# Kernel tuning notes

Measured on AMD Instinct MI355X. Metric: run time of the kernel, lower is better.

## Reference

```python
import jax, jax.numpy as jnp
import numpy as np

COMMIT_WEIGHT = 0.25  # cfg.commit_weight


def setup_inputs() -> dict:
    key = jax.random.key(0)
    k1, k2 = jax.random.split(key)
    z = jax.random.normal(k1, (262144, 64), dtype=jnp.float32)
    codebook = jax.random.normal(k2, (512, 64), dtype=jnp.float32) * 0.02
    return {"z": z, "codebook": codebook}


def reference(z, codebook):
    # projector = Identity (apply_sim_vq=False)
    # squared euclidean distances [N, K]; argmin matches cdist(p=2) argmin
    d2 = (
        jnp.sum(z * z, axis=-1, keepdims=True)
        - 2.0 * (z @ codebook.T)
        + jnp.sum(codebook * codebook, axis=-1)
    )
    ids = jnp.argmin(d2, axis=-1)          # [N] int
    q = codebook[ids]                       # [N, D] gather
    loss = (
        jnp.mean((jax.lax.stop_gradient(z) - q) ** 2)
        + COMMIT_WEIGHT * jnp.mean((jax.lax.stop_gradient(q) - z) ** 2)
    )
    # straight-through estimator (training path)
    q_ste = z + jax.lax.stop_gradient(q - z)
    return q_ste, loss, ids
```

## Files before the change

kernel.cpp:

```cpp
#include <hip/hip_runtime.h>
#include <math.h>


constexpr int D     = 64;
constexpr int D4    = 16;
constexpr int K     = 512;
constexpr float STH = 2e-4f;

typedef __attribute__((ext_vector_type(8)))  short s16x8;
typedef __attribute__((ext_vector_type(16))) float f32x16;

#define FMA4(acc, zz, cc) do { \
  acc = fmaf((zz).x, (cc).x, acc); \
  acc = fmaf((zz).y, (cc).y, acc); \
  acc = fmaf((zz).z, (cc).z, acc); \
  acc = fmaf((zz).w, (cc).w, acc); } while (0)

#define MFMA_B(A, B, C) __builtin_amdgcn_mfma_f32_32x32x16_bf16(A, B, C, 0, 0, 0)

__device__ __forceinline__ unsigned short f2bf(float f) {
  unsigned u = __float_as_uint(f);
  return (unsigned short)((u + 0x7FFFu + ((u >> 16) & 1u)) >> 16);
}


#define LDS_FRAGS(CH, CL, T) do { \
  const int fb_ = (T) * 4096 + h * 512 + col * 16; \
  CH[0] = *(const s16x8*)(smem + fb_); \
  CH[1] = *(const s16x8*)(smem + fb_ + 1024); \
  CH[2] = *(const s16x8*)(smem + fb_ + 2048); \
  CH[3] = *(const s16x8*)(smem + fb_ + 3072); \
  CL[0] = *(const s16x8*)(smem + 65536 + fb_); \
  CL[1] = *(const s16x8*)(smem + 65536 + fb_ + 1024); \
  CL[2] = *(const s16x8*)(smem + 65536 + fb_ + 2048); \
  CL[3] = *(const s16x8*)(smem + 65536 + fb_ + 3072); \
} while (0)

#define LDS_GG(G, T) do { \
  const int gb_ = 131072 + (((T) * 32 + h * 16) << 2); \
  G[0] = *(const float4*)(smem + gb_); \
  G[1] = *(const float4*)(smem + gb_ + 16); \
  G[2] = *(const float4*)(smem + gb_ + 32); \
  G[3] = *(const float4*)(smem + gb_ + 48); \
} while (0)

#define TILE_BODY(T, CH, CL, G) do { \
  f32x16 acc0, acc1 = {};             \
  acc0[0]  = G[0].x; acc0[1]  = G[0].y; acc0[2]  = G[0].z; acc0[3]  = G[0].w; \
  acc0[4]  = G[1].x; acc0[5]  = G[1].y; acc0[6]  = G[1].z; acc0[7]  = G[1].w; \
  acc0[8]  = G[2].x; acc0[9]  = G[2].y; acc0[10] = G[2].z; acc0[11] = G[2].w; \
  acc0[12] = G[3].x; acc0[13] = G[3].y; acc0[14] = G[3].z; acc0[15] = G[3].w; \
  acc0 = MFMA_B(CH[0], zh[0], acc0);  acc1 = MFMA_B(CH[1], zh[1], acc1); \
  acc0 = MFMA_B(CH[2], zh[2], acc0);  acc1 = MFMA_B(CH[3], zh[3], acc1); \
  acc0 = MFMA_B(CH[0], zl[0], acc0);  acc1 = MFMA_B(CH[1], zl[1], acc1); \
  acc0 = MFMA_B(CH[2], zl[2], acc0);  acc1 = MFMA_B(CH[3], zl[3], acc1); \
  acc0 = MFMA_B(CL[0], zh[0], acc0);  acc1 = MFMA_B(CL[1], zh[1], acc1); \
  acc0 = MFMA_B(CL[2], zh[2], acc0);  acc1 = MFMA_B(CL[3], zh[3], acc1); \
  const unsigned m1pre_bits = __float_as_uint(m1); \
  _Pragma("unroll") \
  for (int rp = 0; rp < 8; ++rp) { \
    float va = acc0[2 * rp]     + acc1[2 * rp]; \
    float vb = acc0[2 * rp + 1] + acc1[2 * rp + 1]; \
    va = __uint_as_float((__float_as_uint(va) & 0xFFFFFFF0u) \
                         | (unsigned)(15 - 2 * rp)); \
    vb = __uint_as_float((__float_as_uint(vb) & 0xFFFFFFF0u) \
                         | (unsigned)(14 - 2 * rp)); \
    float tmid = __builtin_amdgcn_fmed3f(va, vb, m1); \
    m1 = fmaxf(fmaxf(va, vb), m1); \
    m2 = fmaxf(m2, tmid); \
  } \
  if (__float_as_uint(m1) != m1pre_bits) tbest = (T); \
} while (0)

__global__ __launch_bounds__(512)
void vq_main(const float* __restrict__ z, const float* __restrict__ cbk,
             float* __restrict__ out, float* __restrict__ lossAcc,
             unsigned* __restrict__ cnt, unsigned* __restrict__ list, int N)
{
  extern __shared__ char smem[];

  const int tid  = threadIdx.x;
  const int lane = tid & 63;
  const int wave = tid >> 6;
  const int col  = lane & 31;
  const int h    = lane >> 5;

  {
    const int cw = tid;
    const float4* c4 = (const float4*)(cbk + (size_t)cw * D);
    const int T = cw >> 5, cc = cw & 31;
    float c2 = 0.f;
    #pragma unroll
    for (int sl = 0; sl < 4; ++sl) {
      float4 f0 = c4[4 * sl];     float4 f1 = c4[4 * sl + 1];
      float4 f2 = c4[4 * sl + 2]; float4 f3 = c4[4 * sl + 3];
      FMA4(c2, f0, f0); FMA4(c2, f1, f1); FMA4(c2, f2, f2); FMA4(c2, f3, f3);
      const float e[16] = {f0.x, f0.y, f0.z, f0.w, f1.x, f1.y, f1.z, f1.w,
                           f2.x, f2.y, f2.z, f2.w, f3.x, f3.y, f3.z, f3.w};
      #pragma unroll
      for (int h2 = 0; h2 < 2; ++h2) {
        s16x8 vh, vl;
        #pragma unroll
        for (int j = 0; j < 8; ++j) {
          unsigned short hb = f2bf(e[h2 * 8 + j]);
          float hf = __uint_as_float((unsigned)hb << 16);
          vh[j] = (short)hb;
          vl[j] = (short)f2bf(e[h2 * 8 + j] - hf);
        }
        const int a = T * 4096 + sl * 1024 + h2 * 512 + cc * 16;
        *(s16x8*)(smem + a) = vh;
        *(s16x8*)(smem + 65536 + a) = vl;
      }
    }
    const int ai = (T << 5) + (((cc >> 2) & 1) << 4) + ((cc >> 3) << 2) + (cc & 3);
    *(float*)(smem + 131072 + ai * 4) = -0.5f * c2;
  }
  __syncthreads();

  float lacc = 0.f;

  #pragma unroll 1
  for (int it = 0; it < 4; ++it) {
    const long rowg = (long)blockIdx.x * 1024 + it * 256 + wave * 32 + col;

    const float4* zp4 = (const float4*)(z + (size_t)rowg * D);
    s16x8 zh[4], zl[4];
    #pragma unroll
    for (int s = 0; s < 4; ++s) {
      float4 p0 = zp4[4 * s + 2 * h];
      float4 p1 = zp4[4 * s + 2 * h + 1];
      float e[8] = {p0.x, p0.y, p0.z, p0.w, p1.x, p1.y, p1.z, p1.w};
      #pragma unroll
      for (int j = 0; j < 8; ++j) {
        unsigned short hb = f2bf(e[j]);
        float hf = __uint_as_float((unsigned)hb << 16);
        zh[s][j] = (short)hb;
        zl[s][j] = (short)f2bf(e[j] - hf);
      }
    }

    float m1 = -INFINITY, m2 = -INFINITY;
    int tbest = 0;

    s16x8 chA[4], clA[4], chB[4], clB[4];
    float4 gA[4], gB[4];
    LDS_FRAGS(chA, clA, 0);  LDS_GG(gA, 0);
    LDS_FRAGS(chB, clB, 1);  LDS_GG(gB, 1);
    #pragma unroll 1
    for (int t = 0; t < 14; t += 2) {
      TILE_BODY(t, chA, clA, gA);
      LDS_FRAGS(chA, clA, t + 2);  LDS_GG(gA, t + 2);
      TILE_BODY(t + 1, chB, clB, gB);
      LDS_FRAGS(chB, clB, t + 3);  LDS_GG(gB, t + 3);
    }
    TILE_BODY(14, chA, clA, gA);
    TILE_BODY(15, chB, clB, gB);

    const int rbest = 15 - (int)(__float_as_uint(m1) & 15u);
    int idx = (tbest << 5) + (h << 2) + (rbest & 3) + ((rbest >> 2) << 3);

    float om1  = __shfl_xor(m1, 32);
    float om2  = __shfl_xor(m2, 32);
    int   oidx = __shfl_xor(idx, 32);
    float nm2 = fmaxf(fminf(m1, om1), fmaxf(m2, om2));
    bool take = (om1 > m1) || ((om1 == m1) && (oidx < idx));
    if (take) { m1 = om1; idx = oidx; }
    m2 = nm2;

    if (m1 - m2 > STH) {
      const float4* qp = (const float4*)(cbk + (size_t)idx * D) + (h << 3);
      const float4* zp = (const float4*)(z + (size_t)rowg * D) + (h << 3);
      float4*       op = (float4*)(out + (size_t)rowg * D) + (h << 3);
      #pragma unroll
      for (int i = 0; i < 8; ++i) {
        float4 q = qp[i], zz = zp[i], u, qs;
        u.x = q.x - zz.x; u.y = q.y - zz.y; u.z = q.z - zz.z; u.w = q.w - zz.w;
        qs.x = zz.x + u.x; qs.y = zz.y + u.y; qs.z = zz.z + u.z; qs.w = zz.w + u.w;
        FMA4(lacc, u, u);
        op[i] = qs;
      }
      if (h == 0) (out + (size_t)N * D + 1)[rowg] = (float)idx;
    } else if (h == 0) {
      unsigned p = atomicAdd(cnt, 1u);
      list[p] = (unsigned)rowg;
    }
  }

  #pragma unroll
  for (int off = 32; off > 0; off >>= 1) lacc += __shfl_down(lacc, off, 64);
  if (lane == 0) atomicAdd(lossAcc, lacc);
}

__global__ __launch_bounds__(256)
void vq_fb(const float* __restrict__ z, const float* __restrict__ cbk,
           float* __restrict__ out, float* __restrict__ lossAcc,
           const unsigned* __restrict__ list, const unsigned* __restrict__ cntp,
           unsigned* __restrict__ done, int N)
{
  const unsigned cnt = *cntp;
  const int tid  = threadIdx.x;
  const int lane = tid & 63;
  const unsigned wid = (blockIdx.x * blockDim.x + tid) >> 6;
  const unsigned nw  = (gridDim.x * blockDim.x) >> 6;

  float lacc = 0.f;
  #pragma unroll 1
  for (unsigned p = wid; p < cnt; p += nw) {
    const size_t r0 = (size_t)list[p];

    const float4* zp = (const float4*)(z + r0 * D);
    float4 z0[D4];
    #pragma unroll
    for (int i = 0; i < D4; ++i) z0[i] = zp[i];
    float z2 = 0.f;
    #pragma unroll
    for (int i = 0; i < D4; ++i) FMA4(z2, z0[i], z0[i]);

    float best = INFINITY;
    int   bi = 0;
    #pragma unroll 1
    for (int j = 0; j < 8; ++j) {
      const int k = (lane << 3) + j;
      const float4* c4 = (const float4*)(cbk + (size_t)k * D);
      float4 cr[D4];
      #pragma unroll
      for (int i = 0; i < D4; ++i) cr[i] = c4[i];
      float c2 = 0.f;
      #pragma unroll
      for (int i = 0; i < D4; ++i) FMA4(c2, cr[i], cr[i]);
      float a0 = 0.f, b0 = 0.f;
      #pragma unroll
      for (int i = 0; i < 8; ++i) {
        FMA4(a0, z0[2 * i],     cr[2 * i]);
        FMA4(b0, z0[2 * i + 1], cr[2 * i + 1]);
      }
      float dot = a0 + b0;
      float d = fmaf(-2.f, dot, z2) + c2;
      if (d < best) { best = d; bi = k; }
    }

    #pragma unroll
    for (int off = 32; off > 0; off >>= 1) {
      float ob = __shfl_xor(best, off, 64);
      int  obi = __shfl_xor(bi, off, 64);
      if (ob < best || (ob == best && obi < bi)) { best = ob; bi = obi; }
    }

    if (lane == 0) {
      const float4* qp = (const float4*)(cbk + (size_t)bi * D);
      float4* o = (float4*)(out + r0 * D);
      #pragma unroll
      for (int i = 0; i < D4; ++i) {
        float4 q = qp[i], zz = z0[i], u, qs;
        u.x = q.x - zz.x; u.y = q.y - zz.y; u.z = q.z - zz.z; u.w = q.w - zz.w;
        qs.x = zz.x + u.x; qs.y = zz.y + u.y; qs.z = zz.z + u.z; qs.w = zz.w + u.w;
        FMA4(lacc, u, u);
        o[i] = qs;
      }
      (out + (size_t)N * D + 1)[r0] = (float)bi;
    }
  }

  #pragma unroll
  for (int off = 32; off > 0; off >>= 1) lacc += __shfl_down(lacc, off, 64);
  __shared__ float wsum[4];
  if (lane == 0) wsum[tid >> 6] = lacc;
  __syncthreads();
  if (tid == 0) {
    float s = wsum[0] + wsum[1] + wsum[2] + wsum[3];
    if (s != 0.f) atomicAdd(lossAcc, s);
    __threadfence();
    unsigned d = atomicAdd(done, 1u);
    if (d == gridDim.x - 1) {
      float total = atomicAdd(lossAcc, 0.0f);
      out[(size_t)N * D] = 1.25f * (total / (float)((long)N * D));
    }
  }
}

extern "C" void kernel_launch(void* const* d_in, const int* in_sizes, int n_in,
                              void* d_out, int out_size, void* d_ws, size_t ws_size,
                              hipStream_t stream)
{
  const float* z   = (const float*)d_in[0];
  const float* cbk = (const float*)d_in[1];
  float* out = (float*)d_out;
  float* ws  = (float*)d_ws;
  const int N = in_sizes[0] / D;

  float*    lossAcc = ws;
  unsigned* cnt     = (unsigned*)(ws + 1);
  unsigned* done    = (unsigned*)(ws + 2);
  unsigned* list    = (unsigned*)(ws + 64);

  hipMemsetAsync(ws, 0, 12, stream);
  vq_main<<<N / 1024, 512, 133120, stream>>>(z, cbk, out, lossAcc, cnt, list, N);
  vq_fb<<<512, 256, 0, stream>>>(z, cbk, out, lossAcc, list, cnt, done, N);
}
```

Before: 214.3 us.

## Use 1024-thread blocks, drop LDS double-buffering, split codebook staging per half-row

The main kernel now launches 1024 threads per block, so each block covers its 1024 rows in two iterations instead of four. Each codebook row is staged into LDS by two threads, with the squared norm combined through a shuffle. The register double-buffering of codebook fragments across tiles is removed in favour of a simple per-tile load loop, and the bias accumulator is loaded directly as one vector. This cuts register pressure so more waves can hide LDS and MFMA latency, at the cost of losing explicit prefetch overlap. With 1024 threads the register budget per thread is lower, which risks spills.

```diff
diff --git a/kernel.cpp b/kernel.cpp
--- a/kernel.cpp
+++ b/kernel.cpp
@@ -36,20 +36,9 @@
   CL[3] = *(const s16x8*)(smem + 65536 + fb_ + 3072); \
 } while (0)
 
-#define LDS_GG(G, T) do { \
-  const int gb_ = 131072 + (((T) * 32 + h * 16) << 2); \
-  G[0] = *(const float4*)(smem + gb_); \
-  G[1] = *(const float4*)(smem + gb_ + 16); \
-  G[2] = *(const float4*)(smem + gb_ + 32); \
-  G[3] = *(const float4*)(smem + gb_ + 48); \
-} while (0)
-
-#define TILE_BODY(T, CH, CL, G) do { \
-  f32x16 acc0, acc1 = {};             \
-  acc0[0]  = G[0].x; acc0[1]  = G[0].y; acc0[2]  = G[0].z; acc0[3]  = G[0].w; \
-  acc0[4]  = G[1].x; acc0[5]  = G[1].y; acc0[6]  = G[1].z; acc0[7]  = G[1].w; \
-  acc0[8]  = G[2].x; acc0[9]  = G[2].y; acc0[10] = G[2].z; acc0[11] = G[2].w; \
-  acc0[12] = G[3].x; acc0[13] = G[3].y; acc0[14] = G[3].z; acc0[15] = G[3].w; \
+#define TILE_BODY(T, CH, CL) do { \
+  f32x16 acc0 = *(const f32x16*)(smem + 131072 + (((T) * 32 + h * 16) << 2)); \
+  f32x16 acc1 = {}; \
   acc0 = MFMA_B(CH[0], zh[0], acc0);  acc1 = MFMA_B(CH[1], zh[1], acc1); \
   acc0 = MFMA_B(CH[2], zh[2], acc0);  acc1 = MFMA_B(CH[3], zh[3], acc1); \
   acc0 = MFMA_B(CH[0], zl[0], acc0);  acc1 = MFMA_B(CH[1], zl[1], acc1); \
@@ -72,7 +61,7 @@
   if (__float_as_uint(m1) != m1pre_bits) tbest = (T); \
 } while (0)
 
-__global__ __launch_bounds__(512)
+__global__ __launch_bounds__(1024)
 void vq_main(const float* __restrict__ z, const float* __restrict__ cbk,
              float* __restrict__ out, float* __restrict__ lossAcc,
              unsigned* __restrict__ cnt, unsigned* __restrict__ list, int N)
@@ -86,42 +75,52 @@
   const int h    = lane >> 5;
 
   {
-    const int cw = tid;
-    const float4* c4 = (const float4*)(cbk + (size_t)cw * D);
+    const int cw   = tid >> 1;
+    const int half = tid & 1;
+    const float4* c4 = (const float4*)(cbk + (size_t)cw * D) + half * 8;
+    float4 f[8];
+    #pragma unroll
+    for (int i = 0; i < 8; ++i) f[i] = c4[i];
+    float pc2 = 0.f;
+    #pragma unroll
+    for (int i = 0; i < 8; ++i) FMA4(pc2, f[i], f[i]);
+    float e[32];
+    #pragma unroll
+    for (int i = 0; i < 8; ++i) {
+      e[4*i] = f[i].x; e[4*i+1] = f[i].y; e[4*i+2] = f[i].z; e[4*i+3] = f[i].w;
+    }
     const int T = cw >> 5, cc = cw & 31;
-    float c2 = 0.f;
-    #pragma unroll
-    for (int sl = 0; sl < 4; ++sl) {
-      float4 f0 = c4[4 * sl];     float4 f1 = c4[4 * sl + 1];
-      float4 f2 = c4[4 * sl + 2]; float4 f3 = c4[4 * sl + 3];
-      FMA4(c2, f0, f0); FMA4(c2, f1, f1); FMA4(c2, f2, f2); FMA4(c2, f3, f3);
-      const float e[16] = {f0.x, f0.y, f0.z, f0.w, f1.x, f1.y, f1.z, f1.w,
-                           f2.x, f2.y, f2.z, f2.w, f3.x, f3.y, f3.z, f3.w};
+    #pragma unroll
+    for (int sl = 0; sl < 2; ++sl) {
       #pragma unroll
       for (int h2 = 0; h2 < 2; ++h2) {
+        const int ld0 = sl * 16 + h2 * 8;
         s16x8 vh, vl;
         #pragma unroll
         for (int j = 0; j < 8; ++j) {
-          unsigned short hb = f2bf(e[h2 * 8 + j]);
+          unsigned short hb = f2bf(e[ld0 + j]);
           float hf = __uint_as_float((unsigned)hb << 16);
           vh[j] = (short)hb;
-          vl[j] = (short)f2bf(e[h2 * 8 + j] - hf);
+          vl[j] = (short)f2bf(e[ld0 + j] - hf);
         }
-        const int a = T * 4096 + sl * 1024 + h2 * 512 + cc * 16;
+        const int a = T * 4096 + (2 * half + sl) * 1024 + h2 * 512 + cc * 16;
         *(s16x8*)(smem + a) = vh;
         *(s16x8*)(smem + 65536 + a) = vl;
       }
     }
-    const int ai = (T << 5) + (((cc >> 2) & 1) << 4) + ((cc >> 3) << 2) + (cc & 3);
-    *(float*)(smem + 131072 + ai * 4) = -0.5f * c2;
+    float c2full = pc2 + __shfl_xor(pc2, 1, 64);
+    if (half == 0) {
+      const int ai = (T << 5) + (((cc >> 2) & 1) << 4) + ((cc >> 3) << 2) + (cc & 3);
+      *(float*)(smem + 131072 + ai * 4) = -0.5f * c2full;
+    }
   }
   __syncthreads();
 
   float lacc = 0.f;
 
   #pragma unroll 1
-  for (int it = 0; it < 4; ++it) {
-    const long rowg = (long)blockIdx.x * 1024 + it * 256 + wave * 32 + col;
+  for (int it = 0; it < 2; ++it) {
+    const long rowg = (long)blockIdx.x * 1024 + it * 512 + wave * 32 + col;
 
     const float4* zp4 = (const float4*)(z + (size_t)rowg * D);
     s16x8 zh[4], zl[4];
@@ -142,19 +141,12 @@
     float m1 = -INFINITY, m2 = -INFINITY;
     int tbest = 0;
 
-    s16x8 chA[4], clA[4], chB[4], clB[4];
-    float4 gA[4], gB[4];
-    LDS_FRAGS(chA, clA, 0);  LDS_GG(gA, 0);
-    LDS_FRAGS(chB, clB, 1);  LDS_GG(gB, 1);
     #pragma unroll 1
-    for (int t = 0; t < 14; t += 2) {
-      TILE_BODY(t, chA, clA, gA);
-      LDS_FRAGS(chA, clA, t + 2);  LDS_GG(gA, t + 2);
-      TILE_BODY(t + 1, chB, clB, gB);
-      LDS_FRAGS(chB, clB, t + 3);  LDS_GG(gB, t + 3);
-    }
-    TILE_BODY(14, chA, clA, gA);
-    TILE_BODY(15, chB, clB, gB);
+    for (int t = 0; t < 16; ++t) {
+      s16x8 ch[4], cl[4];
+      LDS_FRAGS(ch, cl, t);
+      TILE_BODY(t, ch, cl);
+    }
 
     const int rbest = 15 - (int)(__float_as_uint(m1) & 15u);
     int idx = (tbest << 5) + (h << 2) + (rbest & 3) + ((rbest >> 2) << 3);
@@ -294,6 +286,6 @@
   unsigned* list    = (unsigned*)(ws + 64);
 
   hipMemsetAsync(ws, 0, 12, stream);
-  vq_main<<<N / 1024, 512, 133120, stream>>>(z, cbk, out, lossAcc, cnt, list, N);
+  vq_main<<<N / 1024, 1024, 133120, stream>>>(z, cbk, out, lossAcc, cnt, list, N);
   vq_fb<<<512, 256, 0, stream>>>(z, cbk, out, lossAcc, list, cnt, done, N);
 }
```

Result: slower. 221.7 us (+3.5%).
